# Kernel tuning notes

Measured on AMD Instinct MI355X. Metric: run time of the kernel, lower is better.

The kernel has to match this reference:

```python
import jax, jax.numpy as jnp
import numpy as np

RES = 0.5  # voxels.resolution
N_VOX = 65536
M_PTS = 2048


def quaternion_matrix(quat, tran):
    # quat normalized with sqrt(2/|q|^2), then 4x4 outer product Q = q q^T
    q = quat * jnp.sqrt(2.0 / jnp.sum(quat ** 2))
    Q = jnp.outer(q, q)
    R = jnp.array([
        [1.0 - Q[2, 2] - Q[3, 3], Q[1, 2] - Q[3, 0],       Q[1, 3] + Q[2, 0],       tran[0]],
        [Q[1, 2] + Q[3, 0],       1.0 - Q[1, 1] - Q[3, 3], Q[2, 3] - Q[1, 0],       tran[1]],
        [Q[1, 3] - Q[2, 0],       Q[2, 3] + Q[1, 0],       1.0 - Q[1, 1] - Q[2, 2], tran[2]],
        [0.0,                     0.0,                     0.0,                     1.0]],
        dtype=quat.dtype)
    return R


def setup_inputs() -> dict:
    key = jax.random.key(0)
    ks = jax.random.split(key, 8)
    quat = jax.random.normal(ks[0], (4,), jnp.float32)
    tran = jax.random.normal(ks[1], (3,), jnp.float32) * 0.1
    model = jax.random.normal(ks[2], (M_PTS, 3), jnp.float32) * 0.5
    view_matrix = jnp.eye(4, dtype=jnp.float32) + 0.05 * jax.random.normal(ks[3], (4, 4), jnp.float32)
    centers = jax.random.uniform(ks[4], (N_VOX, 3), jnp.float32, -1.0, 1.0)
    free = jax.random.uniform(ks[5], (N_VOX,), jnp.float32)
    occupied_by_other = jax.random.uniform(ks[6], (N_VOX,), jnp.float32)
    masks = (jax.random.uniform(ks[7], (N_VOX,), jnp.float32) < 0.3).astype(jnp.float32)
    return {"quat": quat, "tran": tran, "model": model, "view_matrix": view_matrix,
            "centers": centers, "free": free, "occupied_by_other": occupied_by_other,
            "masks": masks}


def reference(quat, tran, model, view_matrix, centers, free, occupied_by_other, masks):
    mat_eye = quaternion_matrix(quat, tran)                       # (4,4)
    mat_world = jnp.linalg.inv(view_matrix) @ mat_eye             # (4,4)
    model_h = jnp.concatenate([model, jnp.ones((model.shape[0], 1), model.dtype)], 1).T  # (4,M)
    pred = mat_world @ model_h                                    # (4,M)
    pred = (pred / pred[3])[:3].T                                 # (M,3)

    # pairwise distances in voxel coordinates: ||(pred - center)/RES||
    c = centers / RES                                             # (N,3)
    p = pred / RES                                                # (M,3)
    d2 = (jnp.sum(c * c, axis=1)[:, None]
          + jnp.sum(p * p, axis=1)[None, :]
          - 2.0 * (c @ p.T))                                      # (N,M)
    dmin = jnp.sqrt(jnp.maximum(jnp.min(d2, axis=1), 0.0))        # (N,)
    dmin = jnp.minimum(dmin, RES / 2.0)                           # clamp max
    # occupand > 0 write, else stays 0 -> relu (occupand is already >= 0)
    occupied_by_pred = jnp.maximum(1.0 - dmin / (RES / 2.0), 0.0)

    pred_sum = occupied_by_pred.sum()
    mask_sum = masks.sum()
    t1 = jnp.where(pred_sum > 0,
                   ((free + occupied_by_other) * occupied_by_pred).sum()
                   / jnp.where(pred_sum > 0, pred_sum, 1.0), 0.0)
    t2 = jnp.where(mask_sum > 0,
                   (masks * occupied_by_pred).sum()
                   / jnp.where(mask_sum > 0, mask_sum, 1.0), 0.0)
    return t1 - t2
```

## Files before the change

### kernel.cpp

```cpp
#include <hip/hip_runtime.h>
#include <math.h>

#define M_PTS   2048
#define N_VOX   65536
#define VPT     4
#define VPB     256
#define NBLK    (N_VOX / VPB)
#define NWAVES  16
#define CHUNK   (M_PTS / NWAVES)


__global__ __launch_bounds__(1024) void k_fused(const float* __restrict__ quat,
                                                const float* __restrict__ tran,
                                                const float* __restrict__ model,
                                                const float* __restrict__ view,
                                                const float* __restrict__ centers,
                                                const float* __restrict__ freev,
                                                const float* __restrict__ occ_other,
                                                const float* __restrict__ masks,
                                                float* __restrict__ partial) {
    __shared__ float4 sp[M_PTS];
    __shared__ float  pmin[NWAVES * VPB];
    __shared__ float  sred[16];

    const int tid = threadIdx.x;

    float W[16];
    {
        float q0 = quat[0], q1 = quat[1], q2 = quat[2], q3 = quat[3];
        float nq = q0*q0 + q1*q1 + q2*q2 + q3*q3;
        float s = sqrtf(2.0f / nq);
        q0 *= s; q1 *= s; q2 *= s; q3 *= s;
        float E[16];
        E[0]  = 1.0f - q2*q2 - q3*q3; E[1]  = q1*q2 - q3*q0;        E[2]  = q1*q3 + q2*q0;        E[3]  = tran[0];
        E[4]  = q1*q2 + q3*q0;        E[5]  = 1.0f - q1*q1 - q3*q3; E[6]  = q2*q3 - q1*q0;        E[7]  = tran[1];
        E[8]  = q1*q3 - q2*q0;        E[9]  = q2*q3 + q1*q0;        E[10] = 1.0f - q1*q1 - q2*q2; E[11] = tran[2];
        E[12] = 0.0f; E[13] = 0.0f; E[14] = 0.0f; E[15] = 1.0f;

        float m[16], inv[16];
        #pragma unroll
        for (int i = 0; i < 16; i++) m[i] = view[i];

        inv[0]  =  m[5]*m[10]*m[15] - m[5]*m[11]*m[14] - m[9]*m[6]*m[15] + m[9]*m[7]*m[14] + m[13]*m[6]*m[11] - m[13]*m[7]*m[10];
        inv[4]  = -m[4]*m[10]*m[15] + m[4]*m[11]*m[14] + m[8]*m[6]*m[15] - m[8]*m[7]*m[14] - m[12]*m[6]*m[11] + m[12]*m[7]*m[10];
        inv[8]  =  m[4]*m[9]*m[15]  - m[4]*m[11]*m[13] - m[8]*m[5]*m[15] + m[8]*m[7]*m[13] + m[12]*m[5]*m[11] - m[12]*m[7]*m[9];
        inv[12] = -m[4]*m[9]*m[14]  + m[4]*m[10]*m[13] + m[8]*m[5]*m[14] - m[8]*m[6]*m[13] - m[12]*m[5]*m[10] + m[12]*m[6]*m[9];
        inv[1]  = -m[1]*m[10]*m[15] + m[1]*m[11]*m[14] + m[9]*m[2]*m[15] - m[9]*m[3]*m[14] - m[13]*m[2]*m[11] + m[13]*m[3]*m[10];
        inv[5]  =  m[0]*m[10]*m[15] - m[0]*m[11]*m[14] - m[8]*m[2]*m[15] + m[8]*m[3]*m[14] + m[12]*m[2]*m[11] - m[12]*m[3]*m[10];
        inv[9]  = -m[0]*m[9]*m[15]  + m[0]*m[11]*m[13] + m[8]*m[1]*m[15] - m[8]*m[3]*m[13] - m[12]*m[1]*m[11] + m[12]*m[3]*m[9];
        inv[13] =  m[0]*m[9]*m[14]  - m[0]*m[10]*m[13] - m[8]*m[1]*m[14] + m[8]*m[2]*m[13] + m[12]*m[1]*m[10] - m[12]*m[2]*m[9];
        inv[2]  =  m[1]*m[6]*m[15]  - m[1]*m[7]*m[14]  - m[5]*m[2]*m[15] + m[5]*m[3]*m[14] + m[13]*m[2]*m[7]  - m[13]*m[3]*m[6];
        inv[6]  = -m[0]*m[6]*m[15]  + m[0]*m[7]*m[14]  + m[4]*m[2]*m[15] - m[4]*m[3]*m[14] - m[12]*m[2]*m[7]  + m[12]*m[3]*m[6];
        inv[10] =  m[0]*m[5]*m[15]  - m[0]*m[7]*m[13]  - m[4]*m[1]*m[15] + m[4]*m[3]*m[13] + m[12]*m[1]*m[7]  - m[12]*m[3]*m[5];
        inv[14] = -m[0]*m[5]*m[14]  + m[0]*m[6]*m[13]  + m[4]*m[1]*m[14] - m[4]*m[2]*m[13] - m[12]*m[1]*m[6]  + m[12]*m[2]*m[5];
        inv[3]  = -m[1]*m[6]*m[11]  + m[1]*m[7]*m[10]  + m[5]*m[2]*m[11] - m[5]*m[3]*m[10] - m[9]*m[2]*m[7]   + m[9]*m[3]*m[6];
        inv[7]  =  m[0]*m[6]*m[11]  - m[0]*m[7]*m[10]  - m[4]*m[2]*m[11] + m[4]*m[3]*m[10] + m[8]*m[2]*m[7]   - m[8]*m[3]*m[6];
        inv[11] = -m[0]*m[5]*m[11]  + m[0]*m[7]*m[9]   + m[4]*m[1]*m[11] - m[4]*m[3]*m[9]  - m[8]*m[1]*m[7]   + m[8]*m[3]*m[5];
        inv[15] =  m[0]*m[5]*m[10]  - m[0]*m[6]*m[9]   - m[4]*m[1]*m[10] + m[4]*m[2]*m[9]  + m[8]*m[1]*m[6]   - m[8]*m[2]*m[5];

        float det = m[0]*inv[0] + m[1]*inv[4] + m[2]*inv[8] + m[3]*inv[12];
        float rdet = 1.0f / det;

        #pragma unroll
        for (int r = 0; r < 4; r++) {
            #pragma unroll
            for (int c = 0; c < 4; c++) {
                float a = 0.0f;
                #pragma unroll
                for (int k = 0; k < 4; k++) a += inv[4*r+k] * rdet * E[4*k+c];
                W[4*r+c] = a;
            }
        }
    }

    #pragma unroll
    for (int i = tid; i < M_PTS; i += 1024) {
        float x = model[3*i + 0];
        float y = model[3*i + 1];
        float z = model[3*i + 2];
        float X  = W[0]*x + W[1]*y + W[2]*z  + W[3];
        float Y  = W[4]*x + W[5]*y + W[6]*z  + W[7];
        float Z  = W[8]*x + W[9]*y + W[10]*z + W[11];
        float Wd = W[12]*x + W[13]*y + W[14]*z + W[15];
        float rw = 2.0f / Wd;
        float px = X * rw, py = Y * rw, pz = Z * rw;
        float h  = 0.5f * (px*px + py*py + pz*pz);
        sp[i] = make_float4(px, py, pz, h);
    }
    __syncthreads();

    const int lane = tid & 63;
    const int wave = tid >> 6;
    const int vbase = blockIdx.x * VPB + lane * VPT;

    float nx[VPT], ny[VPT], nz[VPT], mm[VPT];
    #pragma unroll
    for (int k = 0; k < VPT; k++) {
        int g = vbase + k;
        nx[k] = -centers[3*g + 0] * 2.0f;
        ny[k] = -centers[3*g + 1] * 2.0f;
        nz[k] = -centers[3*g + 2] * 2.0f;
        mm[k] = 1e30f;
    }

    const float4* base = sp + wave * CHUNK;
    #pragma unroll 4
    for (int j = 0; j < CHUNK; ++j) {
        float4 p = base[j];
        #pragma unroll
        for (int k = 0; k < VPT; k++)
            mm[k] = fminf(mm[k], fmaf(nx[k], p.x, fmaf(ny[k], p.y, fmaf(nz[k], p.z, p.w))));
    }
    #pragma unroll
    for (int k = 0; k < VPT; k++)
        pmin[wave * VPB + lane * VPT + k] = mm[k];
    __syncthreads();

    if (tid < VPB) {
        const int g = blockIdx.x * VPB + tid;
        float m = 1e30f;
        #pragma unroll
        for (int c = 0; c < NWAVES; c++)
            m = fminf(m, pmin[c * VPB + tid]);
        float cx = centers[3*g + 0] * 2.0f;
        float cy = centers[3*g + 1] * 2.0f;
        float cz = centers[3*g + 2] * 2.0f;
        float c2 = cx*cx + cy*cy + cz*cz;
        float d2 = fmaf(2.0f, m, c2);
        float dmin = fminf(sqrtf(fmaxf(d2, 0.0f)), 0.25f);
        float occ  = fmaxf(1.0f - 4.0f * dmin, 0.0f);

        float mk = masks[g];
        float v0 = occ;
        float v1 = (freev[g] + occ_other[g]) * occ;
        float v2 = mk * occ;
        float v3 = mk;

        #pragma unroll
        for (int off = 32; off > 0; off >>= 1) {
            v0 += __shfl_down(v0, off);
            v1 += __shfl_down(v1, off);
            v2 += __shfl_down(v2, off);
            v3 += __shfl_down(v3, off);
        }
        if (lane == 0) {
            sred[wave*4 + 0] = v0;
            sred[wave*4 + 1] = v1;
            sred[wave*4 + 2] = v2;
            sred[wave*4 + 3] = v3;
        }
    }
    __syncthreads();
    if (tid < 4) {
        float s = sred[tid] + sred[4 + tid] + sred[8 + tid] + sred[12 + tid];
        partial[blockIdx.x * 4 + tid] = s;
    }
}

__global__ __launch_bounds__(256) void k_final(const float* __restrict__ partial,
                                               float* __restrict__ out) {
    __shared__ float sred[16];
    const int tid  = threadIdx.x;
    const int lane = tid & 63;
    const int wave = tid >> 6;

    float4 p = ((const float4*)partial)[tid];
    float v0 = p.x, v1 = p.y, v2 = p.z, v3 = p.w;

    #pragma unroll
    for (int off = 32; off > 0; off >>= 1) {
        v0 += __shfl_down(v0, off);
        v1 += __shfl_down(v1, off);
        v2 += __shfl_down(v2, off);
        v3 += __shfl_down(v3, off);
    }
    if (lane == 0) {
        sred[wave*4 + 0] = v0;
        sred[wave*4 + 1] = v1;
        sred[wave*4 + 2] = v2;
        sred[wave*4 + 3] = v3;
    }
    __syncthreads();
    if (tid == 0) {
        float ps = sred[0] + sred[4] + sred[8]  + sred[12];
        float fo = sred[1] + sred[5] + sred[9]  + sred[13];
        float mo = sred[2] + sred[6] + sred[10] + sred[14];
        float ms = sred[3] + sred[7] + sred[11] + sred[15];
        float t1 = (ps > 0.0f) ? (fo / ps) : 0.0f;
        float t2 = (ms > 0.0f) ? (mo / ms) : 0.0f;
        out[0] = t1 - t2;
    }
}

extern "C" void kernel_launch(void* const* d_in, const int* in_sizes, int n_in,
                              void* d_out, int out_size, void* d_ws, size_t ws_size,
                              hipStream_t stream) {
    const float* quat      = (const float*)d_in[0];
    const float* tran      = (const float*)d_in[1];
    const float* model     = (const float*)d_in[2];
    const float* view      = (const float*)d_in[3];
    const float* centers   = (const float*)d_in[4];
    const float* freev     = (const float*)d_in[5];
    const float* occ_other = (const float*)d_in[6];
    const float* masks     = (const float*)d_in[7];
    float* out     = (float*)d_out;
    float* partial = (float*)d_ws;

    k_fused<<<NBLK, 1024, 0, stream>>>(quat, tran, model, view, centers, freev,
                                       occ_other, masks, partial);
    k_final<<<1, 256, 0, stream>>>(partial, out);
}
```

Before: 83.26 us.

## Fuse final reduction via cooperative grid sync and drop block barrier

Merges the two kernels into one cooperative launch that uses a grid-wide sync before block 0 performs the final reduction, removing a second kernel launch. Each wave now transforms exactly the model points in its own chunk, so the block barrier before the distance loop is removed and waves only read points they wrote. It also hoists the center loads ahead of the matrix setup and processes two points per inner iteration with a paired fmin. Cooperative launch requires all 256 blocks of 1024 threads to be co-resident, and a grid sync can cost more than the launch it replaces.

```diff
diff --git a/kernel.cpp b/kernel.cpp
--- a/kernel.cpp
+++ b/kernel.cpp
@@ -1,4 +1,5 @@
 #include <hip/hip_runtime.h>
+#include <hip/hip_cooperative_groups.h>
 #include <math.h>
 
 #define M_PTS   2048
@@ -9,21 +10,37 @@
 #define NWAVES  16
 #define CHUNK   (M_PTS / NWAVES)
 
-
-__global__ __launch_bounds__(1024) void k_fused(const float* __restrict__ quat,
-                                                const float* __restrict__ tran,
-                                                const float* __restrict__ model,
-                                                const float* __restrict__ view,
-                                                const float* __restrict__ centers,
-                                                const float* __restrict__ freev,
-                                                const float* __restrict__ occ_other,
-                                                const float* __restrict__ masks,
-                                                float* __restrict__ partial) {
+namespace cg = cooperative_groups;
+
+
+__global__ __launch_bounds__(1024) void k_all(const float* __restrict__ quat,
+                                              const float* __restrict__ tran,
+                                              const float* __restrict__ model,
+                                              const float* __restrict__ view,
+                                              const float* __restrict__ centers,
+                                              const float* __restrict__ freev,
+                                              const float* __restrict__ occ_other,
+                                              const float* __restrict__ masks,
+                                              float* __restrict__ partial,
+                                              float* __restrict__ out) {
     __shared__ float4 sp[M_PTS];
     __shared__ float  pmin[NWAVES * VPB];
     __shared__ float  sred[16];
 
-    const int tid = threadIdx.x;
+    const int tid  = threadIdx.x;
+    const int lane = tid & 63;
+    const int wave = tid >> 6;
+
+    const int vbase = blockIdx.x * VPB + lane * VPT;
+    float nx[VPT], ny[VPT], nz[VPT], mm[VPT];
+    #pragma unroll
+    for (int k = 0; k < VPT; k++) {
+        int g = vbase + k;
+        nx[k] = -centers[3*g + 0] * 2.0f;
+        ny[k] = -centers[3*g + 1] * 2.0f;
+        nz[k] = -centers[3*g + 2] * 2.0f;
+        mm[k] = 1e30f;
+    }
 
     float W[16];
     {
@@ -74,7 +91,8 @@
     }
 
     #pragma unroll
-    for (int i = tid; i < M_PTS; i += 1024) {
+    for (int u = 0; u < CHUNK / 64; ++u) {
+        int i = wave * CHUNK + u * 64 + lane;
         float x = model[3*i + 0];
         float y = model[3*i + 1];
         float z = model[3*i + 2];
@@ -87,29 +105,18 @@
         float h  = 0.5f * (px*px + py*py + pz*pz);
         sp[i] = make_float4(px, py, pz, h);
     }
-    __syncthreads();
-
-    const int lane = tid & 63;
-    const int wave = tid >> 6;
-    const int vbase = blockIdx.x * VPB + lane * VPT;
-
-    float nx[VPT], ny[VPT], nz[VPT], mm[VPT];
-    #pragma unroll
-    for (int k = 0; k < VPT; k++) {
-        int g = vbase + k;
-        nx[k] = -centers[3*g + 0] * 2.0f;
-        ny[k] = -centers[3*g + 1] * 2.0f;
-        nz[k] = -centers[3*g + 2] * 2.0f;
-        mm[k] = 1e30f;
-    }
 
     const float4* base = sp + wave * CHUNK;
     #pragma unroll 4
-    for (int j = 0; j < CHUNK; ++j) {
-        float4 p = base[j];
-        #pragma unroll
-        for (int k = 0; k < VPT; k++)
-            mm[k] = fminf(mm[k], fmaf(nx[k], p.x, fmaf(ny[k], p.y, fmaf(nz[k], p.z, p.w))));
+    for (int j = 0; j < CHUNK; j += 2) {
+        float4 p0 = base[j];
+        float4 p1 = base[j + 1];
+        #pragma unroll
+        for (int k = 0; k < VPT; k++) {
+            float t0 = fmaf(nx[k], p0.x, fmaf(ny[k], p0.y, fmaf(nz[k], p0.z, p0.w)));
+            float t1 = fmaf(nx[k], p1.x, fmaf(ny[k], p1.y, fmaf(nz[k], p1.z, p1.w)));
+            mm[k] = fminf(mm[k], fminf(t0, t1));
+        }
     }
     #pragma unroll
     for (int k = 0; k < VPT; k++)
@@ -151,44 +158,42 @@
         }
     }
     __syncthreads();
-    if (tid < 4) {
-        float s = sred[tid] + sred[4 + tid] + sred[8 + tid] + sred[12 + tid];
-        partial[blockIdx.x * 4 + tid] = s;
-    }
-}
-
-__global__ __launch_bounds__(256) void k_final(const float* __restrict__ partial,
-                                               float* __restrict__ out) {
-    __shared__ float sred[16];
-    const int tid  = threadIdx.x;
-    const int lane = tid & 63;
-    const int wave = tid >> 6;
-
-    float4 p = ((const float4*)partial)[tid];
-    float v0 = p.x, v1 = p.y, v2 = p.z, v3 = p.w;
-
-    #pragma unroll
-    for (int off = 32; off > 0; off >>= 1) {
-        v0 += __shfl_down(v0, off);
-        v1 += __shfl_down(v1, off);
-        v2 += __shfl_down(v2, off);
-        v3 += __shfl_down(v3, off);
-    }
-    if (lane == 0) {
-        sred[wave*4 + 0] = v0;
-        sred[wave*4 + 1] = v1;
-        sred[wave*4 + 2] = v2;
-        sred[wave*4 + 3] = v3;
-    }
-    __syncthreads();
-    if (tid == 0) {
-        float ps = sred[0] + sred[4] + sred[8]  + sred[12];
-        float fo = sred[1] + sred[5] + sred[9]  + sred[13];
-        float mo = sred[2] + sred[6] + sred[10] + sred[14];
-        float ms = sred[3] + sred[7] + sred[11] + sred[15];
-        float t1 = (ps > 0.0f) ? (fo / ps) : 0.0f;
-        float t2 = (ms > 0.0f) ? (mo / ms) : 0.0f;
-        out[0] = t1 - t2;
+    if (tid < 4)
+        partial[blockIdx.x * 4 + tid] = sred[tid] + sred[4 + tid] + sred[8 + tid] + sred[12 + tid];
+
+    __threadfence();
+    cg::this_grid().sync();
+
+    if (blockIdx.x == 0) {
+        __threadfence();
+        float v0 = 0.0f, v1 = 0.0f, v2 = 0.0f, v3 = 0.0f;
+        if (tid < 256) {
+            float4 p = ((const float4*)partial)[tid];
+            v0 = p.x; v1 = p.y; v2 = p.z; v3 = p.w;
+        }
+        #pragma unroll
+        for (int off = 32; off > 0; off >>= 1) {
+            v0 += __shfl_down(v0, off);
+            v1 += __shfl_down(v1, off);
+            v2 += __shfl_down(v2, off);
+            v3 += __shfl_down(v3, off);
+        }
+        if (tid < 256 && lane == 0) {
+            sred[wave*4 + 0] = v0;
+            sred[wave*4 + 1] = v1;
+            sred[wave*4 + 2] = v2;
+            sred[wave*4 + 3] = v3;
+        }
+        __syncthreads();
+        if (tid == 0) {
+            float ps = sred[0] + sred[4] + sred[8]  + sred[12];
+            float fo = sred[1] + sred[5] + sred[9]  + sred[13];
+            float mo = sred[2] + sred[6] + sred[10] + sred[14];
+            float ms = sred[3] + sred[7] + sred[11] + sred[15];
+            float t1 = (ps > 0.0f) ? (fo / ps) : 0.0f;
+            float t2 = (ms > 0.0f) ? (mo / ms) : 0.0f;
+            out[0] = t1 - t2;
+        }
     }
 }
 
@@ -206,7 +211,8 @@
     float* out     = (float*)d_out;
     float* partial = (float*)d_ws;
 
-    k_fused<<<NBLK, 1024, 0, stream>>>(quat, tran, model, view, centers, freev,
-                                       occ_other, masks, partial);
-    k_final<<<1, 256, 0, stream>>>(partial, out);
+    void* args[10] = {(void*)&quat, (void*)&tran, (void*)&model, (void*)&view,
+                      (void*)&centers, (void*)&freev, (void*)&occ_other,
+                      (void*)&masks, (void*)&partial, (void*)&out};
+    hipLaunchCooperativeKernel(k_all, dim3(NBLK), dim3(1024), args, 0u, stream);
 }
```

Result: slower. 181.7 us (+118.3%).

## Split point set across block pairs and raise voxels per thread to eight

Applied to the files above, without the earlier changes.

The fused kernel is split in two. A min-distance kernel has each pair of blocks handle one 512-voxel group, with each block transforming and scanning half of the model points. Each thread now tracks 8 voxels and reads two points per iteration, so every LDS point load is reused across more FMAs and there is more independent work in flight. Per-half minima go to a workspace buffer, and a separate occupancy kernel combines them and computes the partial sums. Each wave only reads the LDS points it wrote itself, so no barrier is needed before the scan. The cost is an extra kernel launch plus a global round trip for the 2×N minima, and 8 voxels per thread raises register pressure.

```diff
diff --git a/kernel.cpp b/kernel.cpp
--- a/kernel.cpp
+++ b/kernel.cpp
@@ -1,29 +1,41 @@
 #include <hip/hip_runtime.h>
 #include <math.h>
 
-#define M_PTS   2048
-#define N_VOX   65536
-#define VPT     4
-#define VPB     256
-#define NBLK    (N_VOX / VPB)
-#define NWAVES  16
-#define CHUNK   (M_PTS / NWAVES)
-
-
-__global__ __launch_bounds__(1024) void k_fused(const float* __restrict__ quat,
-                                                const float* __restrict__ tran,
-                                                const float* __restrict__ model,
-                                                const float* __restrict__ view,
-                                                const float* __restrict__ centers,
-                                                const float* __restrict__ freev,
-                                                const float* __restrict__ occ_other,
-                                                const float* __restrict__ masks,
-                                                float* __restrict__ partial) {
-    __shared__ float4 sp[M_PTS];
-    __shared__ float  pmin[NWAVES * VPB];
-    __shared__ float  sred[16];
-
-    const int tid = threadIdx.x;
+#define M_PTS    2048
+#define N_VOX    65536
+#define VPT      8
+#define VGRP     512
+#define NGRP     (N_VOX / VGRP)
+#define HALF_PTS 1024
+#define K1_BLK   256
+#define K1_WAVES 16
+#define K1_CHUNK (HALF_PTS / K1_WAVES)
+
+
+__global__ __launch_bounds__(1024) void k_min(const float* __restrict__ quat,
+                                              const float* __restrict__ tran,
+                                              const float* __restrict__ model,
+                                              const float* __restrict__ view,
+                                              const float* __restrict__ centers,
+                                              float* __restrict__ pm) {
+    __shared__ float4 sp[HALF_PTS];
+    __shared__ float  pmin[K1_WAVES][VGRP];
+
+    const int tid  = threadIdx.x;
+    const int lane = tid & 63;
+    const int wave = tid >> 6;
+    const int g    = blockIdx.x >> 1;
+    const int hb   = blockIdx.x & 1;
+
+    float nx[VPT], ny[VPT], nz[VPT], mm[VPT];
+    #pragma unroll
+    for (int k = 0; k < VPT; k++) {
+        int gv = g * VGRP + k * 64 + lane;
+        nx[k] = -centers[3*gv + 0] * 2.0f;
+        ny[k] = -centers[3*gv + 1] * 2.0f;
+        nz[k] = -centers[3*gv + 2] * 2.0f;
+        mm[k] = 1e30f;
+    }
 
     float W[16];
     {
@@ -73,88 +85,90 @@
         }
     }
 
-    #pragma unroll
-    for (int i = tid; i < M_PTS; i += 1024) {
-        float x = model[3*i + 0];
-        float y = model[3*i + 1];
-        float z = model[3*i + 2];
+    {
+        const int ip = hb * HALF_PTS + tid;
+        float x = model[3*ip + 0];
+        float y = model[3*ip + 1];
+        float z = model[3*ip + 2];
         float X  = W[0]*x + W[1]*y + W[2]*z  + W[3];
         float Y  = W[4]*x + W[5]*y + W[6]*z  + W[7];
         float Z  = W[8]*x + W[9]*y + W[10]*z + W[11];
         float Wd = W[12]*x + W[13]*y + W[14]*z + W[15];
         float rw = 2.0f / Wd;
         float px = X * rw, py = Y * rw, pz = Z * rw;
-        float h  = 0.5f * (px*px + py*py + pz*pz);
-        sp[i] = make_float4(px, py, pz, h);
-    }
+        float hh = 0.5f * (px*px + py*py + pz*pz);
+        sp[tid] = make_float4(px, py, pz, hh);
+    }
+
+    const float4* base = sp + wave * K1_CHUNK;
+    #pragma unroll 4
+    for (int j = 0; j < K1_CHUNK; j += 2) {
+        float4 p0 = base[j];
+        float4 p1 = base[j + 1];
+        #pragma unroll
+        for (int k = 0; k < VPT; k++) {
+            float t0 = fmaf(nx[k], p0.x, fmaf(ny[k], p0.y, fmaf(nz[k], p0.z, p0.w)));
+            float t1 = fmaf(nx[k], p1.x, fmaf(ny[k], p1.y, fmaf(nz[k], p1.z, p1.w)));
+            mm[k] = fminf(mm[k], fminf(t0, t1));
+        }
+    }
+    #pragma unroll
+    for (int k = 0; k < VPT; k++)
+        pmin[wave][k * 64 + lane] = mm[k];
     __syncthreads();
 
+    if (tid < VGRP) {
+        float m = 1e30f;
+        #pragma unroll
+        for (int c = 0; c < K1_WAVES; c++)
+            m = fminf(m, pmin[c][tid]);
+        pm[hb * N_VOX + g * VGRP + tid] = m;
+    }
+}
+
+__global__ __launch_bounds__(256) void k_occ(const float* __restrict__ centers,
+                                             const float* __restrict__ freev,
+                                             const float* __restrict__ occ_other,
+                                             const float* __restrict__ masks,
+                                             const float* __restrict__ pm,
+                                             float* __restrict__ partial) {
+    __shared__ float sred[16];
+    const int tid  = threadIdx.x;
     const int lane = tid & 63;
     const int wave = tid >> 6;
-    const int vbase = blockIdx.x * VPB + lane * VPT;
-
-    float nx[VPT], ny[VPT], nz[VPT], mm[VPT];
-    #pragma unroll
-    for (int k = 0; k < VPT; k++) {
-        int g = vbase + k;
-        nx[k] = -centers[3*g + 0] * 2.0f;
-        ny[k] = -centers[3*g + 1] * 2.0f;
-        nz[k] = -centers[3*g + 2] * 2.0f;
-        mm[k] = 1e30f;
-    }
-
-    const float4* base = sp + wave * CHUNK;
-    #pragma unroll 4
-    for (int j = 0; j < CHUNK; ++j) {
-        float4 p = base[j];
-        #pragma unroll
-        for (int k = 0; k < VPT; k++)
-            mm[k] = fminf(mm[k], fmaf(nx[k], p.x, fmaf(ny[k], p.y, fmaf(nz[k], p.z, p.w))));
-    }
-    #pragma unroll
-    for (int k = 0; k < VPT; k++)
-        pmin[wave * VPB + lane * VPT + k] = mm[k];
+    const int v    = blockIdx.x * 256 + tid;
+
+    float m  = fminf(pm[v], pm[N_VOX + v]);
+    float cx = centers[3*v + 0] * 2.0f;
+    float cy = centers[3*v + 1] * 2.0f;
+    float cz = centers[3*v + 2] * 2.0f;
+    float c2 = cx*cx + cy*cy + cz*cz;
+    float d2 = fmaf(2.0f, m, c2);
+    float dmin = fminf(sqrtf(fmaxf(d2, 0.0f)), 0.25f);
+    float occ  = fmaxf(1.0f - 4.0f * dmin, 0.0f);
+
+    float mk = masks[v];
+    float v0 = occ;
+    float v1 = (freev[v] + occ_other[v]) * occ;
+    float v2 = mk * occ;
+    float v3 = mk;
+
+    #pragma unroll
+    for (int off = 32; off > 0; off >>= 1) {
+        v0 += __shfl_down(v0, off);
+        v1 += __shfl_down(v1, off);
+        v2 += __shfl_down(v2, off);
+        v3 += __shfl_down(v3, off);
+    }
+    if (lane == 0) {
+        sred[wave*4 + 0] = v0;
+        sred[wave*4 + 1] = v1;
+        sred[wave*4 + 2] = v2;
+        sred[wave*4 + 3] = v3;
+    }
     __syncthreads();
-
-    if (tid < VPB) {
-        const int g = blockIdx.x * VPB + tid;
-        float m = 1e30f;
-        #pragma unroll
-        for (int c = 0; c < NWAVES; c++)
-            m = fminf(m, pmin[c * VPB + tid]);
-        float cx = centers[3*g + 0] * 2.0f;
-        float cy = centers[3*g + 1] * 2.0f;
-        float cz = centers[3*g + 2] * 2.0f;
-        float c2 = cx*cx + cy*cy + cz*cz;
-        float d2 = fmaf(2.0f, m, c2);
-        float dmin = fminf(sqrtf(fmaxf(d2, 0.0f)), 0.25f);
-        float occ  = fmaxf(1.0f - 4.0f * dmin, 0.0f);
-
-        float mk = masks[g];
-        float v0 = occ;
-        float v1 = (freev[g] + occ_other[g]) * occ;
-        float v2 = mk * occ;
-        float v3 = mk;
-
-        #pragma unroll
-        for (int off = 32; off > 0; off >>= 1) {
-            v0 += __shfl_down(v0, off);
-            v1 += __shfl_down(v1, off);
-            v2 += __shfl_down(v2, off);
-            v3 += __shfl_down(v3, off);
-        }
-        if (lane == 0) {
-            sred[wave*4 + 0] = v0;
-            sred[wave*4 + 1] = v1;
-            sred[wave*4 + 2] = v2;
-            sred[wave*4 + 3] = v3;
-        }
-    }
-    __syncthreads();
-    if (tid < 4) {
-        float s = sred[tid] + sred[4 + tid] + sred[8 + tid] + sred[12 + tid];
-        partial[blockIdx.x * 4 + tid] = s;
-    }
+    if (tid < 4)
+        partial[blockIdx.x * 4 + tid] = sred[tid] + sred[4 + tid] + sred[8 + tid] + sred[12 + tid];
 }
 
 __global__ __launch_bounds__(256) void k_final(const float* __restrict__ partial,
@@ -204,9 +218,10 @@
     const float* occ_other = (const float*)d_in[6];
     const float* masks     = (const float*)d_in[7];
     float* out     = (float*)d_out;
-    float* partial = (float*)d_ws;
-
-    k_fused<<<NBLK, 1024, 0, stream>>>(quat, tran, model, view, centers, freev,
-                                       occ_other, masks, partial);
+    float* pm      = (float*)d_ws;
+    float* partial = pm + 2 * N_VOX;
+
+    k_min<<<K1_BLK, 1024, 0, stream>>>(quat, tran, model, view, centers, pm);
+    k_occ<<<256, 256, 0, stream>>>(centers, freev, occ_other, masks, pm, partial);
     k_final<<<1, 256, 0, stream>>>(partial, out);
 }
```

Result: slower. 87.71 us (+5.3%).
